# Kernel tuning notes

Measured on AMD Instinct MI355X. Metric: run time of the kernel, lower is better.

## Reference

```python
import jax, jax.numpy as jnp
import numpy as np

H = 16
D_MODEL = 1024
D_K = D_MODEL // H


def setup_inputs() -> dict:
    key = jax.random.key(0)
    ks = jax.random.split(key, 11)
    B, S, D = 2, 2048, D_MODEL
    sc = 1.0 / np.sqrt(D)
    return {
        "query": jax.random.normal(ks[0], (B, S, D), jnp.float32),
        "key": jax.random.normal(ks[1], (B, S, D), jnp.float32),
        "value": jax.random.normal(ks[2], (B, S, D), jnp.float32),
        "Wq": jax.random.normal(ks[3], (D, D), jnp.float32) * sc,
        "bq": jnp.zeros((D,), jnp.float32),
        "Wk": jax.random.normal(ks[4], (D, D), jnp.float32) * sc,
        "bk": jnp.zeros((D,), jnp.float32),
        "Wv": jax.random.normal(ks[5], (D, D), jnp.float32) * sc,
        "bv": jnp.zeros((D,), jnp.float32),
        "Wo": jax.random.normal(ks[6], (D, D), jnp.float32) * sc,
        "bo": jnp.zeros((D,), jnp.float32),
    }


def _split_heads(x, B, S):
    # [B,S,D] -> [B,H,S,d_k]
    return x.reshape(B, S, H, D_K).transpose(0, 2, 1, 3)


def reference(query, key, value, Wq, bq, Wk, bk, Wv, bv, Wo, bo):
    B, S, D = query.shape
    q = _split_heads(query @ Wq + bq, B, S)
    k = _split_heads(key @ Wk + bk, B, key.shape[1])
    v = _split_heads(value @ Wv + bv, B, value.shape[1])
    scores = jnp.einsum("bhqd,bhkd->bhqk", q, k) / jnp.sqrt(jnp.asarray(D_K, q.dtype))
    p_attn = jax.nn.softmax(scores, axis=-1)  # dropout is identity at inference
    x = jnp.einsum("bhqk,bhkd->bhqd", p_attn, v)
    x = x.transpose(0, 2, 1, 3).reshape(B, S, H * D_K)
    return x @ Wo + bo
```

## Files before the change

kernel.cpp:

```cpp
#include <hip/hip_runtime.h>

typedef unsigned short u16;
typedef unsigned int   u32;
typedef __bf16 bf16x8 __attribute__((ext_vector_type(8)));
typedef float  f32x4  __attribute__((ext_vector_type(4)));

__device__ __forceinline__ u16 f2bf(float f) {
  u32 u = __float_as_uint(f);
  u += 0x7fffu + ((u >> 16) & 1u);
  return (u16)(u >> 16);
}

__device__ __forceinline__ u32 cvt_pk_bf16(float a, float b) {
  u32 r;
  asm("v_cvt_pk_bf16_f32 %0, %1, %2" : "=v"(r) : "v"(a), "v"(b));
  return r;
}

__device__ __forceinline__ void gll16(const void* g, void* l) {
  __builtin_amdgcn_global_load_lds(
      (__attribute__((address_space(1))) unsigned int*)(g),
      (__attribute__((address_space(3))) unsigned int*)(l), 16, 0, 0);
}

__device__ __forceinline__ void cvt8(const float* __restrict__ s, u16* __restrict__ d, int o) {
  float4 a = *(const float4*)(s + o);
  float4 b = *(const float4*)(s + o + 4);
  uint4 r;
  r.x = cvt_pk_bf16(a.x, a.y);
  r.y = cvt_pk_bf16(a.z, a.w);
  r.z = cvt_pk_bf16(b.x, b.y);
  r.w = cvt_pk_bf16(b.z, b.w);
  *(uint4*)(d + o) = r;
}

__global__ __launch_bounds__(256) void convert_in(
    const float* __restrict__ q, const float* __restrict__ k, const float* __restrict__ v,
    u16* __restrict__ qo, u16* __restrict__ ko, u16* __restrict__ vo) {
  int t = blockIdx.x * 256 + threadIdx.x;
  int o = t * 8;
  cvt8(q, qo, o);
  cvt8(k, ko, o);
  cvt8(v, vo, o);
}

__global__ __launch_bounds__(256) void convert_w(
    const float* __restrict__ Wq, const float* __restrict__ Wk,
    const float* __restrict__ Wv, const float* __restrict__ Wo,
    u16* __restrict__ Wqt, u16* __restrict__ Wkt,
    u16* __restrict__ Wvt, u16* __restrict__ Wot) {
  __shared__ __align__(16) u16 t[64][72];
  int z = blockIdx.z;
  const float* W = (z == 0) ? Wq : (z == 1) ? Wk : (z == 2) ? Wv : Wo;
  u16* Wt = (z == 0) ? Wqt : (z == 1) ? Wkt : (z == 2) ? Wvt : Wot;
  int k0 = blockIdx.y * 64, n0 = blockIdx.x * 64;
  int tid = threadIdx.x;
#pragma unroll
  for (int e = 0; e < 4; ++e) {
    int i = e * 256 + tid;
    int r = i >> 4, c4 = (i & 15) * 4;
    float4 vv = *(const float4*)(W + (size_t)(k0 + r) * 1024 + n0 + c4);
    union { u16 u[4]; uint2 w2; } p;
    p.u[0] = f2bf(vv.x); p.u[1] = f2bf(vv.y); p.u[2] = f2bf(vv.z); p.u[3] = f2bf(vv.w);
    *(uint2*)&t[r][c4] = p.w2;
  }
  __syncthreads();
#pragma unroll
  for (int e = 0; e < 2; ++e) {
    int i = e * 256 + tid;
    int rn = i >> 3, c8 = (i & 7) * 8;
    union { u16 u[8]; uint4 w4; } p;
#pragma unroll
    for (int kk = 0; kk < 8; ++kk) p.u[kk] = t[c8 + kk][rn];
    *(uint4*)(Wt + (size_t)(n0 + rn) * 1024 + k0 + c8) = p.w4;
  }
}

__device__ __forceinline__ void gemm_core(
    const u16* __restrict__ A,
    const u16* __restrict__ Bt,
    int K, int m0, int n0,
    u16* As, u16* Bs, f32x4 acc[4][4]) {
  const int tid = threadIdx.x;
  const int l = tid & 63;
  const int g = l >> 4, q16 = l & 15;
  const int wv = tid >> 6;
  const int wr = wv >> 1, wc = wv & 1;
#pragma unroll
  for (int mi = 0; mi < 4; ++mi)
#pragma unroll
    for (int ni = 0; ni < 4; ++ni) acc[mi][ni] = (f32x4){0.f, 0.f, 0.f, 0.f};

  for (int k0 = 0; k0 < K; k0 += 64) {
    __syncthreads();
#pragma unroll
    for (int c = 0; c < 4; ++c) {
      int i = c * 256 + tid;
      int row = i >> 3, ce = (i & 7) * 8;
      gll16(A + (size_t)(m0 + row) * K + k0 + ce, As + i * 8);
      gll16(Bt + (size_t)(n0 + row) * K + k0 + ce, Bs + i * 8);
    }
    __syncthreads();
#pragma unroll
    for (int kb = 0; kb < 2; ++kb) {
      bf16x8 af[4], bfr[4];
#pragma unroll
      for (int mi = 0; mi < 4; ++mi)
        af[mi] = *(const bf16x8*)(As + (wr * 64 + mi * 16 + q16) * 64 + kb * 32 + g * 8);
#pragma unroll
      for (int ni = 0; ni < 4; ++ni)
        bfr[ni] = *(const bf16x8*)(Bs + (wc * 64 + ni * 16 + q16) * 64 + kb * 32 + g * 8);
#pragma unroll
      for (int mi = 0; mi < 4; ++mi)
#pragma unroll
        for (int ni = 0; ni < 4; ++ni)
          acc[mi][ni] = __builtin_amdgcn_mfma_f32_16x16x32_bf16(af[mi], bfr[ni], acc[mi][ni], 0, 0, 0);
    }
  }
}

__global__ __launch_bounds__(256) void gemm_qkv(
    const u16* __restrict__ qA, const u16* __restrict__ kA, const u16* __restrict__ vA,
    const u16* __restrict__ qW, const u16* __restrict__ kW, const u16* __restrict__ vW,
    const float* __restrict__ qb, const float* __restrict__ kb2, const float* __restrict__ vb,
    u16* __restrict__ Qh, u16* __restrict__ Kh, u16* __restrict__ Vh, float qscale) {
  __shared__ __align__(16) u16 As[128 * 64];
  __shared__ __align__(16) u16 Bs[128 * 64];
  int z = blockIdx.z;
  const u16* A   = (z == 0) ? qA : (z == 1) ? kA : vA;
  const u16* Bt  = (z == 0) ? qW : (z == 1) ? kW : vW;
  const float* bias = (z == 0) ? qb : (z == 1) ? kb2 : vb;
  u16* out = (z == 0) ? Qh : (z == 1) ? Kh : Vh;
  float scale = (z == 0) ? qscale : 1.0f;
  int m0 = blockIdx.y * 128, n0 = blockIdx.x * 128;
  f32x4 acc[4][4];
  gemm_core(A, Bt, 1024, m0, n0, As, Bs, acc);

  const int tid = threadIdx.x;
  const int l = tid & 63;
  const int g = l >> 4, q16 = l & 15;
  const int wv = tid >> 6;
  const int wr = wv >> 1, wc = wv & 1;
#pragma unroll
  for (int ni = 0; ni < 4; ++ni) {
    int n = n0 + wc * 64 + ni * 16 + q16;
    float bvv = bias[n];
    int hh = n >> 6, dk = n & 63;
#pragma unroll
    for (int mi = 0; mi < 4; ++mi) {
#pragma unroll
      for (int j = 0; j < 4; ++j) {
        int m = m0 + wr * 64 + mi * 16 + g * 4 + j;
        int b = m >> 11, s = m & 2047;
        float v = (acc[mi][ni][j] + bvv) * scale;
        out[(((size_t)b * 16 + hh) * 2048 + s) * 64 + dk] = f2bf(v);
      }
    }
  }
}

__global__ __launch_bounds__(256) void gemm_out(
    const u16* __restrict__ A, const u16* __restrict__ Bt,
    const float* __restrict__ bias, float* __restrict__ Out) {
  __shared__ __align__(16) u16 As[128 * 64];
  __shared__ __align__(16) u16 Bs[128 * 64];
  int m0 = blockIdx.y * 128, n0 = blockIdx.x * 128;
  f32x4 acc[4][4];
  gemm_core(A, Bt, 1024, m0, n0, As, Bs, acc);

  const int tid = threadIdx.x;
  const int l = tid & 63;
  const int g = l >> 4, q16 = l & 15;
  const int wv = tid >> 6;
  const int wr = wv >> 1, wc = wv & 1;
#pragma unroll
  for (int ni = 0; ni < 4; ++ni) {
    int n = n0 + wc * 64 + ni * 16 + q16;
    float bvv = bias[n];
#pragma unroll
    for (int mi = 0; mi < 4; ++mi) {
#pragma unroll
      for (int j = 0; j < 4; ++j) {
        int m = m0 + wr * 64 + mi * 16 + g * 4 + j;
        Out[(size_t)m * 1024 + n] = acc[mi][ni][j] + bvv;
      }
    }
  }
}

__global__ __launch_bounds__(256) void transpose_v(const u16* __restrict__ Vh, u16* __restrict__ Vt) {
  __shared__ __align__(16) u16 t[64][72];
  int bh = blockIdx.y, s0 = blockIdx.x * 64;
  int tid = threadIdx.x;
#pragma unroll
  for (int e = 0; e < 2; ++e) {
    int i = e * 256 + tid;
    int r = i >> 3, c8 = (i & 7) * 8;
    uint4 vv = *(const uint4*)(Vh + ((size_t)bh * 2048 + s0 + r) * 64 + c8);
    *(uint4*)&t[r][c8] = vv;
  }
  __syncthreads();
#pragma unroll
  for (int e = 0; e < 2; ++e) {
    int i = e * 256 + tid;
    int d = i >> 3, s8 = (i & 7) * 8;
    union { u16 u[8]; uint4 w4; } p;
#pragma unroll
    for (int kk = 0; kk < 8; ++kk) p.u[kk] = t[s8 + kk][d];
    *(uint4*)(Vt + ((size_t)bh * 64 + d) * 2048 + s0 + s8) = p.w4;
  }
}

__global__ __launch_bounds__(512) void attn_kernel(
    const u16* __restrict__ Qh,
    const u16* __restrict__ Kh,
    const u16* __restrict__ Vt,
    u16* __restrict__ Xb) {
  __shared__ __align__(16) u16 Ks[2][64 * 64];
  __shared__ __align__(16) u16 Vs[2][64 * 64];
  __shared__ __align__(16) u16 Ps[8][16][72];

  const int tid = threadIdx.x;
  const int l = tid & 63, wv = tid >> 6;
  const int g = l >> 4, q16 = l & 15;
  const int qblk = blockIdx.x, bh = blockIdx.y;
  const int b = bh >> 4, h = bh & 15;
  const int qrow0 = qblk * 128 + wv * 16;

  const int srow = tid >> 3;
  const int sc8  = (tid & 7) ^ (srow & 7);
  const u16* Kbase = Kh + (size_t)bh * 2048 * 64;
  const u16* Vbase = Vt + (size_t)bh * 64 * 2048;

  bf16x8 bq[2];
#pragma unroll
  for (int kb = 0; kb < 2; ++kb)
    bq[kb] = *(const bf16x8*)(Qh + ((size_t)bh * 2048 + qrow0 + q16) * 64 + kb * 32 + g * 8);

  f32x4 x[4];
#pragma unroll
  for (int ni = 0; ni < 4; ++ni) x[ni] = (f32x4){0.f, 0.f, 0.f, 0.f};
  float m_run = -3e38f, l_run = 0.f;

  gll16(Kbase + (size_t)srow * 64 + sc8 * 8, &Ks[0][tid * 8]);
  gll16(Vbase + (size_t)srow * 2048 + sc8 * 8, &Vs[0][tid * 8]);
  asm volatile("s_waitcnt vmcnt(0)" ::: "memory");
  __builtin_amdgcn_s_barrier();

  for (int kt = 0; kt < 32; ++kt) {
    const int cb = kt & 1, nb = cb ^ 1;
    if (kt + 1 < 32) {
      gll16(Kbase + ((size_t)(kt + 1) * 64 + srow) * 64 + sc8 * 8, &Ks[nb][tid * 8]);
      gll16(Vbase + (size_t)srow * 2048 + (kt + 1) * 64 + sc8 * 8, &Vs[nb][tid * 8]);
    }

    f32x4 st[4];
#pragma unroll
    for (int mi = 0; mi < 4; ++mi) st[mi] = (f32x4){0.f, 0.f, 0.f, 0.f};
#pragma unroll
    for (int mi = 0; mi < 4; ++mi) {
      int row = mi * 16 + q16;
#pragma unroll
      for (int kb = 0; kb < 2; ++kb) {
        int pc8 = (kb * 4 + g) ^ (row & 7);
        bf16x8 ak = *(const bf16x8*)(&Ks[cb][row * 64 + pc8 * 8]);
        st[mi] = __builtin_amdgcn_mfma_f32_16x16x32_bf16(ak, bq[kb], st[mi], 0, 0, 0);
      }
    }

    float mx = st[0][0];
#pragma unroll
    for (int mi = 0; mi < 4; ++mi)
#pragma unroll
      for (int j = 0; j < 4; ++j) mx = fmaxf(mx, st[mi][j]);
    mx = fmaxf(mx, __shfl_xor(mx, 16));
    mx = fmaxf(mx, __shfl_xor(mx, 32));

    float mref, sf;
    if (__all(mx <= m_run + 8.f)) {
      mref = m_run; sf = 1.f;
    } else {
      mref = fmaxf(m_run, mx);
      sf = __builtin_amdgcn_exp2f(m_run - mref);
      m_run = mref;
#pragma unroll
      for (int j = 0; j < 4; ++j) {
        float sfx = __shfl(sf, g * 4 + j);
#pragma unroll
        for (int ni = 0; ni < 4; ++ni) x[ni][j] *= sfx;
      }
    }

    float rs = 0.f;
#pragma unroll
    for (int mi = 0; mi < 4; ++mi)
#pragma unroll
      for (int j = 0; j < 4; ++j) {
        float p = __builtin_amdgcn_exp2f(st[mi][j] - mref);
        st[mi][j] = p;
        rs += p;
      }
    rs += __shfl_xor(rs, 16);
    rs += __shfl_xor(rs, 32);
    l_run = l_run * sf + rs;

#pragma unroll
    for (int mi = 0; mi < 4; ++mi) {
      uint2 w;
      w.x = cvt_pk_bf16(st[mi][0], st[mi][1]);
      w.y = cvt_pk_bf16(st[mi][2], st[mi][3]);
      *(uint2*)&Ps[wv][q16][mi * 16 + g * 4] = w;
    }

#pragma unroll
    for (int kkb = 0; kkb < 2; ++kkb) {
      bf16x8 ap = *(const bf16x8*)&Ps[wv][q16][kkb * 32 + g * 8];
#pragma unroll
      for (int ni = 0; ni < 4; ++ni) {
        int d = ni * 16 + q16;
        int pc8 = (kkb * 4 + g) ^ (d & 7);
        bf16x8 vf = *(const bf16x8*)(&Vs[cb][d * 64 + pc8 * 8]);
        x[ni] = __builtin_amdgcn_mfma_f32_16x16x32_bf16(ap, vf, x[ni], 0, 0, 0);
      }
    }

    asm volatile("s_waitcnt vmcnt(0)" ::: "memory");
    __builtin_amdgcn_s_barrier();
  }

  float li = 1.0f / l_run;
#pragma unroll
  for (int j = 0; j < 4; ++j) {
    float lv = __shfl(li, g * 4 + j);
    int srw = b * 2048 + qblk * 128 + wv * 16 + g * 4 + j;
#pragma unroll
    for (int ni = 0; ni < 4; ++ni) {
      int col = h * 64 + ni * 16 + q16;
      Xb[(size_t)srw * 1024 + col] = f2bf(x[ni][j] * lv);
    }
  }
}

extern "C" void kernel_launch(void* const* d_in, const int* in_sizes, int n_in,
                              void* d_out, int out_size, void* d_ws, size_t ws_size,
                              hipStream_t stream) {
  (void)in_sizes; (void)n_in; (void)out_size; (void)ws_size;
  const float* q  = (const float*)d_in[0];
  const float* k  = (const float*)d_in[1];
  const float* v  = (const float*)d_in[2];
  const float* Wq = (const float*)d_in[3];
  const float* bq = (const float*)d_in[4];
  const float* Wk = (const float*)d_in[5];
  const float* bk = (const float*)d_in[6];
  const float* Wv = (const float*)d_in[7];
  const float* bv = (const float*)d_in[8];
  const float* Wo = (const float*)d_in[9];
  const float* bo = (const float*)d_in[10];

  char* W = (char*)d_ws;
  const size_t MB = 1ull << 20;
  u16* qbf = (u16*)(W + 0 * MB);
  u16* kbf = (u16*)(W + 8 * MB);
  u16* vbf = (u16*)(W + 16 * MB);
  u16* wqt = (u16*)(W + 24 * MB);
  u16* wkt = (u16*)(W + 26 * MB);
  u16* wvt = (u16*)(W + 28 * MB);
  u16* wot = (u16*)(W + 30 * MB);
  u16* Qh  = (u16*)(W + 32 * MB);
  u16* Kh  = (u16*)(W + 40 * MB);
  u16* Vh  = (u16*)(W + 48 * MB);
  u16* Vtb = (u16*)(W + 56 * MB);
  u16* Xb  = (u16*)(W + 64 * MB);

  convert_in<<<2048, 256, 0, stream>>>(q, k, v, qbf, kbf, vbf);
  convert_w<<<dim3(16, 16, 4), 256, 0, stream>>>(Wq, Wk, Wv, Wo, wqt, wkt, wvt, wot);
  const float QSCALE = 0.125f * 1.4426950408889634f;
  gemm_qkv<<<dim3(8, 32, 3), 256, 0, stream>>>(qbf, kbf, vbf, wqt, wkt, wvt,
                                               bq, bk, bv, Qh, Kh, Vh, QSCALE);
  transpose_v<<<dim3(32, 32), 256, 0, stream>>>(Vh, Vtb);
  attn_kernel<<<dim3(16, 32), 512, 0, stream>>>(Qh, Kh, Vtb, Xb);
  gemm_out<<<dim3(8, 32), 256, 0, stream>>>(Xb, wot, bo, (float*)d_out);
}
```

Before: 154.3 us.

## Swizzle blocks across XCDs, halve attention block size, add MFMA priority hints

Remaps workgroup IDs in the GEMM and attention kernels so neighbouring tiles land on the same XCD, aiming to improve L2 reuse of shared K/V and weight tiles. The attention kernel moves from 512-thread blocks covering 128 query rows to 256-thread blocks covering 64 rows, with twice as many blocks and a launch-bounds hint for three blocks per CU. It also raises wave priority around the MFMA sections and computes the row max with v_max3. Smaller blocks load each K/V tile twice as often per query row, which adds global and LDS traffic in exchange for more resident blocks and better latency hiding.

```diff
diff --git a/kernel.cpp b/kernel.cpp
--- a/kernel.cpp
+++ b/kernel.cpp
@@ -17,10 +17,21 @@
   return r;
 }
 
+__device__ __forceinline__ float max3f(float a, float b, float c) {
+  float r;
+  asm("v_max3_f32 %0, %1, %2, %3" : "=v"(r) : "v"(a), "v"(b), "v"(c));
+  return r;
+}
+
 __device__ __forceinline__ void gll16(const void* g, void* l) {
   __builtin_amdgcn_global_load_lds(
       (__attribute__((address_space(1))) unsigned int*)(g),
       (__attribute__((address_space(3))) unsigned int*)(l), 16, 0, 0);
+}
+
+__device__ __forceinline__ int xcd_swz(int wg, int nwg) {
+  int cpx = nwg >> 3;
+  return (wg & 7) * cpx + (wg >> 3);
 }
 
 __device__ __forceinline__ void cvt8(const float* __restrict__ s, u16* __restrict__ d, int o) {
@@ -132,7 +143,8 @@
   const float* bias = (z == 0) ? qb : (z == 1) ? kb2 : vb;
   u16* out = (z == 0) ? Qh : (z == 1) ? Kh : Vh;
   float scale = (z == 0) ? qscale : 1.0f;
-  int m0 = blockIdx.y * 128, n0 = blockIdx.x * 128;
+  int swz = xcd_swz(blockIdx.y * gridDim.x + blockIdx.x, gridDim.x * gridDim.y);
+  int m0 = (swz >> 3) * 128, n0 = (swz & 7) * 128;
   f32x4 acc[4][4];
   gemm_core(A, Bt, 1024, m0, n0, As, Bs, acc);
 
@@ -164,7 +176,8 @@
     const float* __restrict__ bias, float* __restrict__ Out) {
   __shared__ __align__(16) u16 As[128 * 64];
   __shared__ __align__(16) u16 Bs[128 * 64];
-  int m0 = blockIdx.y * 128, n0 = blockIdx.x * 128;
+  int swz = xcd_swz(blockIdx.y * gridDim.x + blockIdx.x, gridDim.x * gridDim.y);
+  int m0 = (swz >> 3) * 128, n0 = (swz & 7) * 128;
   f32x4 acc[4][4];
   gemm_core(A, Bt, 1024, m0, n0, As, Bs, acc);
 
@@ -211,24 +224,23 @@
   }
 }
 
-__global__ __launch_bounds__(512) void attn_kernel(
+__global__ __launch_bounds__(256, 3) void attn_kernel(
     const u16* __restrict__ Qh,
     const u16* __restrict__ Kh,
     const u16* __restrict__ Vt,
     u16* __restrict__ Xb) {
   __shared__ __align__(16) u16 Ks[2][64 * 64];
   __shared__ __align__(16) u16 Vs[2][64 * 64];
-  __shared__ __align__(16) u16 Ps[8][16][72];
+  __shared__ __align__(16) u16 Ps[4][16][72];
 
   const int tid = threadIdx.x;
   const int l = tid & 63, wv = tid >> 6;
   const int g = l >> 4, q16 = l & 15;
-  const int qblk = blockIdx.x, bh = blockIdx.y;
+  int swz = xcd_swz(blockIdx.y * gridDim.x + blockIdx.x, gridDim.x * gridDim.y);
+  const int qblk = swz & 31, bh = swz >> 5;
   const int b = bh >> 4, h = bh & 15;
-  const int qrow0 = qblk * 128 + wv * 16;
-
-  const int srow = tid >> 3;
-  const int sc8  = (tid & 7) ^ (srow & 7);
+  const int qrow0 = qblk * 64 + wv * 16;
+
   const u16* Kbase = Kh + (size_t)bh * 2048 * 64;
   const u16* Vbase = Vt + (size_t)bh * 64 * 2048;
 
@@ -242,21 +254,32 @@
   for (int ni = 0; ni < 4; ++ni) x[ni] = (f32x4){0.f, 0.f, 0.f, 0.f};
   float m_run = -3e38f, l_run = 0.f;
 
-  gll16(Kbase + (size_t)srow * 64 + sc8 * 8, &Ks[0][tid * 8]);
-  gll16(Vbase + (size_t)srow * 2048 + sc8 * 8, &Vs[0][tid * 8]);
+#pragma unroll
+  for (int c = 0; c < 2; ++c) {
+    int i = c * 256 + tid;
+    int row = i >> 3, sc8 = (i & 7) ^ (row & 7);
+    gll16(Kbase + (size_t)row * 64 + sc8 * 8, &Ks[0][i * 8]);
+    gll16(Vbase + (size_t)row * 2048 + sc8 * 8, &Vs[0][i * 8]);
+  }
   asm volatile("s_waitcnt vmcnt(0)" ::: "memory");
   __builtin_amdgcn_s_barrier();
 
   for (int kt = 0; kt < 32; ++kt) {
     const int cb = kt & 1, nb = cb ^ 1;
     if (kt + 1 < 32) {
-      gll16(Kbase + ((size_t)(kt + 1) * 64 + srow) * 64 + sc8 * 8, &Ks[nb][tid * 8]);
-      gll16(Vbase + (size_t)srow * 2048 + (kt + 1) * 64 + sc8 * 8, &Vs[nb][tid * 8]);
+#pragma unroll
+      for (int c = 0; c < 2; ++c) {
+        int i = c * 256 + tid;
+        int row = i >> 3, sc8 = (i & 7) ^ (row & 7);
+        gll16(Kbase + ((size_t)(kt + 1) * 64 + row) * 64 + sc8 * 8, &Ks[nb][i * 8]);
+        gll16(Vbase + (size_t)row * 2048 + (kt + 1) * 64 + sc8 * 8, &Vs[nb][i * 8]);
+      }
     }
 
     f32x4 st[4];
 #pragma unroll
     for (int mi = 0; mi < 4; ++mi) st[mi] = (f32x4){0.f, 0.f, 0.f, 0.f};
+    __builtin_amdgcn_s_setprio(1);
 #pragma unroll
     for (int mi = 0; mi < 4; ++mi) {
       int row = mi * 16 + q16;
@@ -267,12 +290,17 @@
         st[mi] = __builtin_amdgcn_mfma_f32_16x16x32_bf16(ak, bq[kb], st[mi], 0, 0, 0);
       }
     }
-
-    float mx = st[0][0];
-#pragma unroll
-    for (int mi = 0; mi < 4; ++mi)
-#pragma unroll
-      for (int j = 0; j < 4; ++j) mx = fmaxf(mx, st[mi][j]);
+    __builtin_amdgcn_s_setprio(0);
+
+    float ma = max3f(st[0][0], st[0][1], st[0][2]);
+    ma = max3f(ma, st[0][3], st[1][0]);
+    ma = max3f(ma, st[1][1], st[1][2]);
+    ma = fmaxf(ma, st[1][3]);
+    float mb = max3f(st[2][0], st[2][1], st[2][2]);
+    mb = max3f(mb, st[2][3], st[3][0]);
+    mb = max3f(mb, st[3][1], st[3][2]);
+    mb = fmaxf(mb, st[3][3]);
+    float mx = fmaxf(ma, mb);
     mx = fmaxf(mx, __shfl_xor(mx, 16));
     mx = fmaxf(mx, __shfl_xor(mx, 32));
 
@@ -312,6 +340,7 @@
       *(uint2*)&Ps[wv][q16][mi * 16 + g * 4] = w;
     }
 
+    __builtin_amdgcn_s_setprio(1);
 #pragma unroll
     for (int kkb = 0; kkb < 2; ++kkb) {
       bf16x8 ap = *(const bf16x8*)&Ps[wv][q16][kkb * 32 + g * 8];
@@ -323,6 +352,7 @@
         x[ni] = __builtin_amdgcn_mfma_f32_16x16x32_bf16(ap, vf, x[ni], 0, 0, 0);
       }
     }
+    __builtin_amdgcn_s_setprio(0);
 
     asm volatile("s_waitcnt vmcnt(0)" ::: "memory");
     __builtin_amdgcn_s_barrier();
@@ -332,7 +362,7 @@
 #pragma unroll
   for (int j = 0; j < 4; ++j) {
     float lv = __shfl(li, g * 4 + j);
-    int srw = b * 2048 + qblk * 128 + wv * 16 + g * 4 + j;
+    int srw = b * 2048 + qblk * 64 + wv * 16 + g * 4 + j;
 #pragma unroll
     for (int ni = 0; ni < 4; ++ni) {
       int col = h * 64 + ni * 16 + q16;
@@ -378,6 +408,6 @@
   gemm_qkv<<<dim3(8, 32, 3), 256, 0, stream>>>(qbf, kbf, vbf, wqt, wkt, wvt,
                                                bq, bk, bv, Qh, Kh, Vh, QSCALE);
   transpose_v<<<dim3(32, 32), 256, 0, stream>>>(Vh, Vtb);
-  attn_kernel<<<dim3(16, 32), 512, 0, stream>>>(Qh, Kh, Vtb, Xb);
+  attn_kernel<<<dim3(32, 32), 256, 0, stream>>>(Qh, Kh, Vtb, Xb);
   gemm_out<<<dim3(8, 32), 256, 0, stream>>>(Xb, wot, bo, (float*)d_out);
 }
```

New measurement: 177.9 us. +15.3%, slower.
